# Optimization experiments

Hardware: AMD Instinct MI355X
Metric: run time of the kernel (lower is better)

## Reference

```python
import jax, jax.numpy as jnp
import numpy as np

N = 20000          # nodes
E = 320000         # edges (before self-loops)
H, C = 8, 32       # heads, hidden_size
ND, ED = 6, 11     # node_dim, edge_dim (hard-coded in module)
HC = H * C
DIFF_SCALE = 100.0
SLOPE = 0.2        # GATv2 leaky_relu negative_slope


def _glorot(k, shape):
    fan_in, fan_out = shape[0], shape[-1]
    lim = float(np.sqrt(6.0 / (fan_in + fan_out)))
    return jax.random.uniform(k, shape, jnp.float32, -lim, lim)


def setup_inputs() -> dict:
    key = jax.random.key(0)
    ks = jax.random.split(key, 16)
    d = {}
    d["x"] = jax.random.normal(ks[0], (N, ND), jnp.float32)
    d["edge_index"] = jax.random.randint(ks[1], (2, E), 0, N)
    d["edge_attr"] = jax.random.normal(ks[2], (E, ED), jnp.float32)
    # layer 0 (node_dim -> H*C, with edge features)
    d["Wl0"] = _glorot(ks[3], (ND, HC)); d["bl0"] = jnp.zeros((HC,), jnp.float32)
    d["Wr0"] = _glorot(ks[4], (ND, HC)); d["br0"] = jnp.zeros((HC,), jnp.float32)
    d["We0"] = _glorot(ks[5], (ED, HC))
    d["att0"] = _glorot(ks[6], (H, C))
    d["bias0"] = jnp.zeros((HC,), jnp.float32)
    # layer 1 (H*C -> H*C, no edge features)
    d["Wl1"] = _glorot(ks[7], (HC, HC)); d["bl1"] = jnp.zeros((HC,), jnp.float32)
    d["Wr1"] = _glorot(ks[8], (HC, HC)); d["br1"] = jnp.zeros((HC,), jnp.float32)
    d["att1"] = _glorot(ks[9], (H, C))
    d["bias1"] = jnp.zeros((HC,), jnp.float32)
    return d


def _gatv2(x, src, tgt, Wl, bl, Wr, br, att, bias, e=None, We=None):
    n = x.shape[0]
    xl = (x @ Wl + bl).reshape(n, H, C)   # source transform (messages)
    xr = (x @ Wr + br).reshape(n, H, C)   # target transform
    m = xl[src] + xr[tgt]                 # [E', H, C]
    if e is not None:
        m = m + (e @ We).reshape(-1, H, C)
    s = jax.nn.leaky_relu(m, SLOPE)
    logits = jnp.einsum('ehc,hc->eh', s, att)            # [E', H]
    # segment softmax over incoming edges of each target node
    mx = jax.ops.segment_max(logits, tgt, num_segments=n)
    ex = jnp.exp(logits - mx[tgt])
    den = jax.ops.segment_sum(ex, tgt, num_segments=n)
    alpha = ex / den[tgt]                                 # [E', H]
    out = jax.ops.segment_sum(alpha[:, :, None] * xl[src], tgt, num_segments=n)
    return out.reshape(n, HC) + bias


def reference(x, edge_index, edge_attr, Wl0, bl0, Wr0, br0, We0, att0, bias0,
              Wl1, bl1, Wr1, br1, att1, bias1):
    # preprocessing from GraphEmbedder.forward
    x = jnp.where((x[:, 2] == 1)[:, None] & (jnp.arange(ND) == 1)[None, :],
                  ((x[:, 1] - x[:, 0]) / DIFF_SCALE)[:, None], x)
    edge_attr = jnp.where((edge_attr[:, -2] == 1)[:, None] & (jnp.arange(ED) == 1)[None, :],
                          ((edge_attr[:, 1] - edge_attr[:, 0]) / DIFF_SCALE)[:, None], edge_attr)
    # add self-loops (PyG GATv2Conv default, fill_value='mean' for edge_attr)
    loop = jnp.arange(N)
    src = jnp.concatenate([edge_index[0], loop])
    tgt = jnp.concatenate([edge_index[1], loop])
    ea = jnp.concatenate([edge_attr, jnp.broadcast_to(edge_attr.mean(0), (N, ED))])
    h = _gatv2(x, src, tgt, Wl0, bl0, Wr0, br0, att0, bias0, e=ea, We=We0)
    h = jax.nn.elu(h)
    h = _gatv2(h, src, tgt, Wl1, bl1, Wr1, br1, att1, bias1)
    return h
```

## Files before the change

kernel.cpp:

```cpp
#include <hip/hip_runtime.h>
#include <cstddef>

#define N_H 8
#define N_C 32
#define N_HC 256
#define SLOPE 0.2f

__global__ __launch_bounds__(256) void ea_colsum_kernel(const float* __restrict__ ea,
                                                        float* __restrict__ sums, int E) {
    float loc[11];
#pragma unroll
    for (int j = 0; j < 11; ++j) loc[j] = 0.f;
    for (int i = blockIdx.x * blockDim.x + threadIdx.x; i < E; i += gridDim.x * blockDim.x) {
        float r[11];
#pragma unroll
        for (int j = 0; j < 11; ++j) r[j] = ea[i * 11 + j];
        if (r[9] == 1.0f) r[1] = (r[1] - r[0]) * 0.01f;
#pragma unroll
        for (int j = 0; j < 11; ++j) loc[j] += r[j];
    }
    __shared__ float sbuf[256];
#pragma unroll
    for (int j = 0; j < 11; ++j) {
        sbuf[threadIdx.x] = loc[j];
        __syncthreads();
        for (int s = 128; s > 0; s >>= 1) {
            if (threadIdx.x < s) sbuf[threadIdx.x] += sbuf[threadIdx.x + s];
            __syncthreads();
        }
        if (threadIdx.x == 0) atomicAdd(&sums[j], sbuf[0]);
        __syncthreads();
    }
}

__global__ void mean_div_kernel(const float* __restrict__ sums, float* __restrict__ mean, int E) {
    int t = threadIdx.x;
    if (t < 11) mean[t] = sums[t] / (float)E;
}

__global__ __launch_bounds__(256) void deg_hist_kernel(const int* __restrict__ ei,
                                                       int* __restrict__ deg, int E, int Etot) {
    int e = blockIdx.x * blockDim.x + threadIdx.x;
    if (e >= Etot) return;
    int t = (e < E) ? ei[E + e] : e - E;
    atomicAdd(&deg[t], 1);
}

__global__ __launch_bounds__(1024) void scan_kernel(const int* __restrict__ deg,
                                                    int* __restrict__ offs,
                                                    int* __restrict__ cursor, int Nn) {
    const int T = 1024;
    int tid = threadIdx.x;
    int chunk = (Nn + T - 1) / T;
    int b = tid * chunk;
    int s = 0;
    for (int k = 0; k < chunk; ++k) {
        int i = b + k;
        if (i < Nn) s += deg[i];
    }
    __shared__ int sm[T];
    sm[tid] = s;
    __syncthreads();
    for (int d = 1; d < T; d <<= 1) {
        int v = (tid >= d) ? sm[tid - d] : 0;
        __syncthreads();
        sm[tid] += v;
        __syncthreads();
    }
    int pref = (tid > 0) ? sm[tid - 1] : 0;
    for (int k = 0; k < chunk; ++k) {
        int i = b + k;
        if (i < Nn) {
            offs[i] = pref;
            cursor[i] = pref;
            pref += deg[i];
        }
    }
    if (tid == T - 1) offs[Nn] = sm[T - 1];
}

__global__ __launch_bounds__(256) void scatter_kernel(const int* __restrict__ ei,
                                                      const float* __restrict__ ea,
                                                      const float* __restrict__ mean_ea,
                                                      int* __restrict__ cursor,
                                                      int* __restrict__ esrc,
                                                      float* __restrict__ ea_csr, int E,
                                                      int Etot) {
    int e = blockIdx.x * blockDim.x + threadIdx.x;
    if (e >= Etot) return;
    int s, t;
    if (e < E) { s = ei[e]; t = ei[E + e]; }
    else       { s = t = e - E; }
    int pos = atomicAdd(&cursor[t], 1);
    esrc[pos] = s;
    float r[11];
    if (e < E) {
#pragma unroll
        for (int j = 0; j < 11; ++j) r[j] = ea[(size_t)e * 11 + j];
        if (r[9] == 1.0f) r[1] = (r[1] - r[0]) * 0.01f;
    } else {
#pragma unroll
        for (int j = 0; j < 11; ++j) r[j] = mean_ea[j];
    }
    float* dst = ea_csr + (size_t)pos * 12;
#pragma unroll
    for (int j = 0; j < 11; ++j) dst[j] = r[j];
}

template <int K, int R>
__global__ __launch_bounds__(256) void node_mm_kernel(const float* __restrict__ X,
                                                      const float* __restrict__ Wl,
                                                      const float* __restrict__ bl,
                                                      const float* __restrict__ Wr,
                                                      const float* __restrict__ br,
                                                      float* __restrict__ xl,
                                                      float* __restrict__ xr, int Nn) {
    __shared__ float xs[R][K];
    int row0 = blockIdx.x * R;
    int tid = threadIdx.x;
    for (int i = tid; i < R * K; i += blockDim.x) {
        int r = i / K, k = i - r * K;
        int gr = row0 + r;
        float v = 0.f;
        if (gr < Nn) {
            v = X[(size_t)gr * K + k];
            if (k == 1) {
                float x0 = X[(size_t)gr * K + 0];
                float x2 = X[(size_t)gr * K + 2];
                if (x2 == 1.0f) v = (v - x0) * 0.01f;
            }
        }
        xs[r][k] = v;
    }
    __syncthreads();
    int c = tid;
    float accl[R], accr[R];
#pragma unroll
    for (int r = 0; r < R; ++r) { accl[r] = bl[c]; accr[r] = br[c]; }
#pragma unroll
    for (int k = 0; k < K; ++k) {
        float wl = Wl[k * N_HC + c], wr = Wr[k * N_HC + c];
#pragma unroll
        for (int r = 0; r < R; ++r) {
            accl[r] = fmaf(xs[r][k], wl, accl[r]);
            accr[r] = fmaf(xs[r][k], wr, accr[r]);
        }
    }
#pragma unroll
    for (int r = 0; r < R; ++r) {
        int gr = row0 + r;
        if (gr < Nn) {
            xl[(size_t)gr * N_HC + c] = accl[r];
            xr[(size_t)gr * N_HC + c] = accr[r];
        }
    }
}

__global__ __launch_bounds__(256) void gemm256_kernel(const float* __restrict__ X,
                                                      const float* __restrict__ Wl,
                                                      const float* __restrict__ bl,
                                                      const float* __restrict__ Wr,
                                                      const float* __restrict__ br,
                                                      float* __restrict__ xl,
                                                      float* __restrict__ xr, int Nn) {
    __shared__ float As[32][128];
    __shared__ float Bs[32][128];

    const int by = blockIdx.y;
    const float* __restrict__ W = (by < 2) ? Wl : Wr;
    const float* __restrict__ bias = (by < 2) ? bl : br;
    float* __restrict__ dst = (by < 2) ? xl : xr;
    const int cb = (by & 1) * 128;
    const int row0 = blockIdx.x * 128;
    const int tid = threadIdx.x;
    const int tx = tid & 15, ty = tid >> 4;
    const int tx4 = tx * 4, ty4 = ty * 4;

    const int arow = tid & 127;
    const int akh = (tid >> 7) * 16;
    const int bk0 = tid >> 5;
    const int bc4 = (tid & 31) * 4;

    float acc[8][8];
#pragma unroll
    for (int i = 0; i < 8; ++i)
#pragma unroll
        for (int j = 0; j < 8; ++j) acc[i][j] = 0.f;

    const int garow = row0 + arow;
    const bool aval = garow < Nn;
    const float* __restrict__ asrc = X + (size_t)garow * 256 + akh;

    for (int s = 0; s < 256; s += 32) {
        float4 av[4];
#pragma unroll
        for (int q = 0; q < 4; ++q)
            av[q] = aval ? *(const float4*)(asrc + s + q * 4)
                         : float4{0.f, 0.f, 0.f, 0.f};
#pragma unroll
        for (int q = 0; q < 4; ++q) {
            As[akh + q * 4 + 0][arow] = av[q].x;
            As[akh + q * 4 + 1][arow] = av[q].y;
            As[akh + q * 4 + 2][arow] = av[q].z;
            As[akh + q * 4 + 3][arow] = av[q].w;
        }
#pragma unroll
        for (int q = 0; q < 4; ++q) {
            int kr = bk0 + q * 8;
            *(float4*)&Bs[kr][bc4] = *(const float4*)(W + (size_t)(s + kr) * 256 + cb + bc4);
        }
        __syncthreads();
#pragma unroll 8
        for (int k = 0; k < 32; ++k) {
            const float4 a0 = *(const float4*)&As[k][ty4];
            const float4 a1 = *(const float4*)&As[k][64 + ty4];
            const float4 b0 = *(const float4*)&Bs[k][tx4];
            const float4 b1 = *(const float4*)&Bs[k][64 + tx4];
            const float ar[8] = {a0.x, a0.y, a0.z, a0.w, a1.x, a1.y, a1.z, a1.w};
            const float brr[8] = {b0.x, b0.y, b0.z, b0.w, b1.x, b1.y, b1.z, b1.w};
#pragma unroll
            for (int i = 0; i < 8; ++i)
#pragma unroll
                for (int j = 0; j < 8; ++j) acc[i][j] = fmaf(ar[i], brr[j], acc[i][j]);
        }
        __syncthreads();
    }

    const float4 bv0 = *(const float4*)(bias + cb + tx4);
    const float4 bv1 = *(const float4*)(bias + cb + 64 + tx4);
#pragma unroll
    for (int i = 0; i < 8; ++i) {
        int r = row0 + ((i < 4) ? (ty4 + i) : (64 + ty4 + i - 4));
        if (r < Nn) {
            float4 v0 = {acc[i][0] + bv0.x, acc[i][1] + bv0.y, acc[i][2] + bv0.z,
                         acc[i][3] + bv0.w};
            float4 v1 = {acc[i][4] + bv1.x, acc[i][5] + bv1.y, acc[i][6] + bv1.z,
                         acc[i][7] + bv1.w};
            *(float4*)(dst + (size_t)r * N_HC + cb + tx4) = v0;
            *(float4*)(dst + (size_t)r * N_HC + cb + 64 + tx4) = v1;
        }
    }
}

__device__ __forceinline__ void online_update(float logit, const float4& xlv, float& m,
                                              float& den, float4& acc) {
    float mn = fmaxf(m, logit);
    float s = __expf(m - mn);
    float w = __expf(logit - mn);
    den = den * s + w;
    acc.x = fmaf(w, xlv.x, acc.x * s);
    acc.y = fmaf(w, xlv.y, acc.y * s);
    acc.z = fmaf(w, xlv.z, acc.z * s);
    acc.w = fmaf(w, xlv.w, acc.w * s);
    m = mn;
}

template <bool L0>
__device__ __forceinline__ float edge_logit(const float4& xlv, const float4& xrv,
                                            const float4* Wreg, const float* __restrict__ eap,
                                            const float4& av) {
    float m0 = xlv.x + xrv.x, m1 = xlv.y + xrv.y, m2 = xlv.z + xrv.z, m3 = xlv.w + xrv.w;
    if (L0) {
#pragma unroll
        for (int j = 0; j < 11; ++j) {
            float aj = eap[j];
            m0 = fmaf(aj, Wreg[j].x, m0);
            m1 = fmaf(aj, Wreg[j].y, m1);
            m2 = fmaf(aj, Wreg[j].z, m2);
            m3 = fmaf(aj, Wreg[j].w, m3);
        }
    }
    m0 = m0 > 0.f ? m0 : SLOPE * m0;
    m1 = m1 > 0.f ? m1 : SLOPE * m1;
    m2 = m2 > 0.f ? m2 : SLOPE * m2;
    m3 = m3 > 0.f ? m3 : SLOPE * m3;
    float p = m0 * av.x + m1 * av.y + m2 * av.z + m3 * av.w;
    p += __shfl_xor(p, 1);
    p += __shfl_xor(p, 2);
    p += __shfl_xor(p, 4);
    return p;
}

template <bool L0>
__global__ __launch_bounds__(256) void node_gather_kernel(
    const int* __restrict__ offs, const int* __restrict__ esrc,
    const float* __restrict__ ea_csr, const float* __restrict__ We,
    const float* __restrict__ att, const float* __restrict__ xl, const float* __restrict__ xr,
    const float* __restrict__ bias, float* __restrict__ out, int Nn) {
    int wid = threadIdx.x >> 6;
    int lane = threadIdx.x & 63;
    int node = blockIdx.x * 4 + wid;
    if (node >= Nn) return;
    int c4 = lane * 4;

    float4 Wreg[11];
    if (L0) {
#pragma unroll
        for (int j = 0; j < 11; ++j) Wreg[j] = *(const float4*)(We + j * N_HC + c4);
    }
    const float4 xrv = *(const float4*)(xr + (size_t)node * N_HC + c4);
    const float4 av = *(const float4*)(att + c4);

    int beg = offs[node], end = offs[node + 1];

    float mA = -INFINITY, dA = 0.f;
    float mB = -INFINITY, dB = 0.f;
    float mC = -INFINITY, dC = 0.f;
    float mD = -INFINITY, dD = 0.f;
    float4 aA = {0.f, 0.f, 0.f, 0.f}, aB = aA, aC = aA, aD = aA;

    int p = beg;
    for (; p + 3 < end; p += 4) {
        int pu = __builtin_amdgcn_readfirstlane(p);
        int s0 = esrc[pu + 0];
        int s1 = esrc[pu + 1];
        int s2 = esrc[pu + 2];
        int s3 = esrc[pu + 3];
        const float4 x0 = *(const float4*)(xl + (size_t)s0 * N_HC + c4);
        const float4 x1 = *(const float4*)(xl + (size_t)s1 * N_HC + c4);
        const float4 x2 = *(const float4*)(xl + (size_t)s2 * N_HC + c4);
        const float4 x3 = *(const float4*)(xl + (size_t)s3 * N_HC + c4);
        const float* e0 = L0 ? (ea_csr + (size_t)(pu + 0) * 12) : nullptr;
        const float* e1 = L0 ? (ea_csr + (size_t)(pu + 1) * 12) : nullptr;
        const float* e2 = L0 ? (ea_csr + (size_t)(pu + 2) * 12) : nullptr;
        const float* e3 = L0 ? (ea_csr + (size_t)(pu + 3) * 12) : nullptr;
        float lg0 = edge_logit<L0>(x0, xrv, Wreg, e0, av);
        float lg1 = edge_logit<L0>(x1, xrv, Wreg, e1, av);
        float lg2 = edge_logit<L0>(x2, xrv, Wreg, e2, av);
        float lg3 = edge_logit<L0>(x3, xrv, Wreg, e3, av);
        online_update(lg0, x0, mA, dA, aA);
        online_update(lg1, x1, mB, dB, aB);
        online_update(lg2, x2, mC, dC, aC);
        online_update(lg3, x3, mD, dD, aD);
    }
    for (; p < end; ++p) {
        int pu = __builtin_amdgcn_readfirstlane(p);
        int s0 = esrc[pu];
        const float4 x0 = *(const float4*)(xl + (size_t)s0 * N_HC + c4);
        const float* e0 = L0 ? (ea_csr + (size_t)pu * 12) : nullptr;
        float lg0 = edge_logit<L0>(x0, xrv, Wreg, e0, av);
        online_update(lg0, x0, mA, dA, aA);
    }

    float mm = fmaxf(fmaxf(mA, mB), fmaxf(mC, mD));
    float sA = __expf(mA - mm), sB = __expf(mB - mm);
    float sC = __expf(mC - mm), sD = __expf(mD - mm);
    float den = dA * sA + dB * sB + dC * sC + dD * sD;
    float4 acct;
    acct.x = aA.x * sA + aB.x * sB + aC.x * sC + aD.x * sD;
    acct.y = aA.y * sA + aB.y * sB + aC.y * sC + aD.y * sD;
    acct.z = aA.z * sA + aB.z * sB + aC.z * sC + aD.z * sD;
    acct.w = aA.w * sA + aB.w * sB + aC.w * sC + aD.w * sD;

    const float4 bv = *(const float4*)(bias + c4);
    float4 r;
    r.x = acct.x / den + bv.x;
    r.y = acct.y / den + bv.y;
    r.z = acct.z / den + bv.z;
    r.w = acct.w / den + bv.w;
    if (L0) {
        r.x = r.x > 0.f ? r.x : (__expf(r.x) - 1.f);
        r.y = r.y > 0.f ? r.y : (__expf(r.y) - 1.f);
        r.z = r.z > 0.f ? r.z : (__expf(r.z) - 1.f);
        r.w = r.w > 0.f ? r.w : (__expf(r.w) - 1.f);
    }
    *(float4*)(out + (size_t)node * N_HC + c4) = r;
}

extern "C" void kernel_launch(void* const* d_in, const int* in_sizes, int n_in, void* d_out,
                              int out_size, void* d_ws, size_t ws_size, hipStream_t stream) {
    const float* x = (const float*)d_in[0];
    const int* ei = (const int*)d_in[1];
    const float* ea = (const float*)d_in[2];
    const float* Wl0 = (const float*)d_in[3];
    const float* bl0 = (const float*)d_in[4];
    const float* Wr0 = (const float*)d_in[5];
    const float* br0 = (const float*)d_in[6];
    const float* We0 = (const float*)d_in[7];
    const float* att0 = (const float*)d_in[8];
    const float* bias0 = (const float*)d_in[9];
    const float* Wl1 = (const float*)d_in[10];
    const float* bl1 = (const float*)d_in[11];
    const float* Wr1 = (const float*)d_in[12];
    const float* br1 = (const float*)d_in[13];
    const float* att1 = (const float*)d_in[14];
    const float* bias1 = (const float*)d_in[15];
    float* out = (float*)d_out;

    const int Nn = in_sizes[0] / 6;
    const int E = in_sizes[1] / 2;
    const int Etot = E + Nn;

    auto align16 = [](size_t v) { return (v + 15) & ~(size_t)15; };
    float* ws = (float*)d_ws;
    size_t o = 0;
    float* xl = ws + o;     o = align16(o + (size_t)Nn * N_HC);
    float* xr = ws + o;     o = align16(o + (size_t)Nn * N_HC);
    float* h = ws + o;      o = align16(o + (size_t)Nn * N_HC);
    float* ea_csr = ws + o; o = align16(o + (size_t)Etot * 12);
    float* easum = ws + o;  o = align16(o + 16);
    float* mean = ws + o;   o = align16(o + 16);
    int* deg = (int*)(ws + o);    o = align16(o + (size_t)Nn);
    int* offs = (int*)(ws + o);   o = align16(o + (size_t)Nn + 1);
    int* cursor = (int*)(ws + o); o = align16(o + (size_t)Nn);
    int* esrc = (int*)(ws + o);   o = align16(o + (size_t)Etot);

    hipMemsetAsync(easum, 0, 16 * sizeof(float), stream);
    hipMemsetAsync(deg, 0, (size_t)Nn * sizeof(int), stream);

    ea_colsum_kernel<<<256, 256, 0, stream>>>(ea, easum, E);
    mean_div_kernel<<<1, 32, 0, stream>>>(easum, mean, E);

    deg_hist_kernel<<<(Etot + 255) / 256, 256, 0, stream>>>(ei, deg, E, Etot);
    scan_kernel<<<1, 1024, 0, stream>>>(deg, offs, cursor, Nn);
    scatter_kernel<<<(Etot + 255) / 256, 256, 0, stream>>>(ei, ea, mean, cursor, esrc, ea_csr, E,
                                                           Etot);

    const int gblocks = (Nn + 3) / 4;

    node_mm_kernel<6, 8><<<(Nn + 7) / 8, 256, 0, stream>>>(x, Wl0, bl0, Wr0, br0, xl, xr, Nn);
    node_gather_kernel<true><<<gblocks, 256, 0, stream>>>(offs, esrc, ea_csr, We0, att0, xl, xr,
                                                          bias0, h, Nn);

    dim3 ggrid((Nn + 127) / 128, 4);
    gemm256_kernel<<<ggrid, 256, 0, stream>>>(h, Wl1, bl1, Wr1, br1, xl, xr, Nn);
    node_gather_kernel<false><<<gblocks, 256, 0, stream>>>(offs, esrc, nullptr, nullptr, att1, xl,
                                                           xr, bias1, out, Nn);
}
```

Measured before the change: 322.8 us.

## Run layer-1 GEMM on bf16 MFMA with split hi/lo precision emulation

Replaces the FP32 SIMT GEMM for the 256x512 layer-1 projection with an MFMA bf16 kernel. Each operand is split into a bf16 high part and a residual low part, and three MFMA products are summed to approximate fp32 accuracy. This adds two conversion kernels and uses the output buffer as scratch for the converted activations. The MFMA kernel loads operands straight from global memory without LDS staging. Accuracy is somewhat below true fp32, and the extra conversion traffic could offset the gain from the faster matrix units.

Measured after the change: 347.4 us. 1.08x slower.

```diff
diff --git a/kernel.cpp b/kernel.cpp
--- a/kernel.cpp
+++ b/kernel.cpp
@@ -5,6 +5,18 @@
 #define N_C 32
 #define N_HC 256
 #define SLOPE 0.2f
+
+typedef __attribute__((ext_vector_type(8))) short short8v;
+typedef __attribute__((ext_vector_type(4))) float f32x4;
+
+__device__ __forceinline__ short f2bf(float f) {
+    unsigned u = __float_as_uint(f);
+    unsigned r = (u + 0x7FFFu + ((u >> 16) & 1u)) >> 16;
+    return (short)r;
+}
+__device__ __forceinline__ float bf2f(short s) {
+    return __uint_as_float(((unsigned)(unsigned short)s) << 16);
+}
 
 __global__ __launch_bounds__(256) void ea_colsum_kernel(const float* __restrict__ ea,
                                                         float* __restrict__ sums, int E) {
@@ -156,6 +168,98 @@
     }
 }
 
+__global__ __launch_bounds__(256) void convert_h_kernel(const float* __restrict__ h,
+                                                        short* __restrict__ Ahi,
+                                                        short* __restrict__ Alo, int n4) {
+    int i = blockIdx.x * blockDim.x + threadIdx.x;
+    if (i >= n4) return;
+    float4 v = ((const float4*)h)[i];
+    short h0 = f2bf(v.x), h1 = f2bf(v.y), h2 = f2bf(v.z), h3 = f2bf(v.w);
+    short4 hv = {h0, h1, h2, h3};
+    short4 lv = {f2bf(v.x - bf2f(h0)), f2bf(v.y - bf2f(h1)), f2bf(v.z - bf2f(h2)),
+                 f2bf(v.w - bf2f(h3))};
+    *(short4*)(Ahi + (size_t)i * 4) = hv;
+    *(short4*)(Alo + (size_t)i * 4) = lv;
+}
+
+__global__ __launch_bounds__(256) void convert_w_kernel(const float* __restrict__ Wl,
+                                                        const float* __restrict__ Wr,
+                                                        short* __restrict__ Bthi,
+                                                        short* __restrict__ Btlo) {
+    int n = blockIdx.x;
+    int k = threadIdx.x;
+    float v = (n < 256) ? Wl[(size_t)k * 256 + n] : Wr[(size_t)k * 256 + (n - 256)];
+    short hi = f2bf(v);
+    short lo = f2bf(v - bf2f(hi));
+    size_t idx = (size_t)n * 256 + k;
+    Bthi[idx] = hi;
+    Btlo[idx] = lo;
+}
+
+__global__ __launch_bounds__(256) void gemm_mfma_kernel(
+    const short* __restrict__ Ahi, const short* __restrict__ Alo,
+    const short* __restrict__ Bthi, const short* __restrict__ Btlo,
+    const float* __restrict__ bl, const float* __restrict__ br, float* __restrict__ xl,
+    float* __restrict__ xr, int Nn) {
+    const int wid = threadIdx.x >> 6, lane = threadIdx.x & 63;
+    const int lm = lane & 15, lg = lane >> 4;
+    const int r0 = blockIdx.x * 128 + wid * 32;
+    const int c0 = blockIdx.y * 64;
+    const int kg = lg * 8;
+
+    f32x4 acc[2][4];
+#pragma unroll
+    for (int i = 0; i < 2; ++i)
+#pragma unroll
+        for (int j = 0; j < 4; ++j) acc[i][j] = {0.f, 0.f, 0.f, 0.f};
+
+    const int rA0 = r0 + lm, rA1 = r0 + 16 + lm;
+    const bool v0 = rA0 < Nn, v1 = rA1 < Nn;
+    const short* pa0h = Ahi + (size_t)rA0 * 256 + kg;
+    const short* pa0l = Alo + (size_t)rA0 * 256 + kg;
+    const short* pa1h = Ahi + (size_t)rA1 * 256 + kg;
+    const short* pa1l = Alo + (size_t)rA1 * 256 + kg;
+    const size_t nb = (size_t)(c0 + lm) * 256 + kg;
+    const short8v zz = (short8v)0;
+
+    for (int k0 = 0; k0 < 256; k0 += 32) {
+        short8v a0h = v0 ? *(const short8v*)(pa0h + k0) : zz;
+        short8v a0l = v0 ? *(const short8v*)(pa0l + k0) : zz;
+        short8v a1h = v1 ? *(const short8v*)(pa1h + k0) : zz;
+        short8v a1l = v1 ? *(const short8v*)(pa1l + k0) : zz;
+#pragma unroll
+        for (int ni = 0; ni < 4; ++ni) {
+            const short8v bh = *(const short8v*)(Bthi + nb + (size_t)ni * 16 * 256 + k0);
+            const short8v blo = *(const short8v*)(Btlo + nb + (size_t)ni * 16 * 256 + k0);
+            acc[0][ni] = __builtin_amdgcn_mfma_f32_16x16x32_bf16(a0h, bh, acc[0][ni], 0, 0, 0);
+            acc[0][ni] = __builtin_amdgcn_mfma_f32_16x16x32_bf16(a0l, bh, acc[0][ni], 0, 0, 0);
+            acc[0][ni] = __builtin_amdgcn_mfma_f32_16x16x32_bf16(a0h, blo, acc[0][ni], 0, 0, 0);
+            acc[1][ni] = __builtin_amdgcn_mfma_f32_16x16x32_bf16(a1h, bh, acc[1][ni], 0, 0, 0);
+            acc[1][ni] = __builtin_amdgcn_mfma_f32_16x16x32_bf16(a1l, bh, acc[1][ni], 0, 0, 0);
+            acc[1][ni] = __builtin_amdgcn_mfma_f32_16x16x32_bf16(a1h, blo, acc[1][ni], 0, 0, 0);
+        }
+    }
+
+    const bool left = (c0 < 256);
+    const float* __restrict__ bias = left ? bl : br;
+    float* __restrict__ dst = left ? xl : xr;
+    const int cl = (c0 & 255) + lm;
+#pragma unroll
+    for (int ni = 0; ni < 4; ++ni) {
+        int col = cl + ni * 16;
+        float bv = bias[col];
+#pragma unroll
+        for (int mi = 0; mi < 2; ++mi) {
+            int rb = r0 + mi * 16 + lg * 4;
+#pragma unroll
+            for (int e = 0; e < 4; ++e) {
+                int row = rb + e;
+                if (row < Nn) dst[(size_t)row * N_HC + col] = acc[mi][ni][e] + bv;
+            }
+        }
+    }
+}
+
 __global__ __launch_bounds__(256) void gemm256_kernel(const float* __restrict__ X,
                                                       const float* __restrict__ Wl,
                                                       const float* __restrict__ bl,
@@ -195,8 +299,7 @@
         float4 av[4];
 #pragma unroll
         for (int q = 0; q < 4; ++q)
-            av[q] = aval ? *(const float4*)(asrc + s + q * 4)
-                         : float4{0.f, 0.f, 0.f, 0.f};
+            av[q] = aval ? *(const float4*)(asrc + s + q * 4) : float4{0.f, 0.f, 0.f, 0.f};
 #pragma unroll
         for (int q = 0; q < 4; ++q) {
             As[akh + q * 4 + 0][arow] = av[q].x;
@@ -232,12 +335,12 @@
     for (int i = 0; i < 8; ++i) {
         int r = row0 + ((i < 4) ? (ty4 + i) : (64 + ty4 + i - 4));
         if (r < Nn) {
-            float4 v0 = {acc[i][0] + bv0.x, acc[i][1] + bv0.y, acc[i][2] + bv0.z,
+            float4 u0 = {acc[i][0] + bv0.x, acc[i][1] + bv0.y, acc[i][2] + bv0.z,
                          acc[i][3] + bv0.w};
-            float4 v1 = {acc[i][4] + bv1.x, acc[i][5] + bv1.y, acc[i][6] + bv1.z,
+            float4 u1 = {acc[i][4] + bv1.x, acc[i][5] + bv1.y, acc[i][6] + bv1.z,
                          acc[i][7] + bv1.w};
-            *(float4*)(dst + (size_t)r * N_HC + cb + tx4) = v0;
-            *(float4*)(dst + (size_t)r * N_HC + cb + 64 + tx4) = v1;
+            *(float4*)(dst + (size_t)r * N_HC + cb + tx4) = u0;
+            *(float4*)(dst + (size_t)r * N_HC + cb + 64 + tx4) = u1;
         }
     }
 }
@@ -404,6 +507,9 @@
     int* offs = (int*)(ws + o);   o = align16(o + (size_t)Nn + 1);
     int* cursor = (int*)(ws + o); o = align16(o + (size_t)Nn);
     int* esrc = (int*)(ws + o);   o = align16(o + (size_t)Etot);
+    short* Bthi = (short*)(ws + o); o = align16(o + 512 * 256 / 2);
+    short* Btlo = (short*)(ws + o); o = align16(o + 512 * 256 / 2);
+    const bool use_mfma = (o * sizeof(float) <= ws_size);
 
     hipMemsetAsync(easum, 0, 16 * sizeof(float), stream);
     hipMemsetAsync(deg, 0, (size_t)Nn * sizeof(int), stream);
@@ -422,8 +528,18 @@
     node_gather_kernel<true><<<gblocks, 256, 0, stream>>>(offs, esrc, ea_csr, We0, att0, xl, xr,
                                                           bias0, h, Nn);
 
-    dim3 ggrid((Nn + 127) / 128, 4);
-    gemm256_kernel<<<ggrid, 256, 0, stream>>>(h, Wl1, bl1, Wr1, br1, xl, xr, Nn);
+    if (use_mfma) {
+        short* Ahi = (short*)d_out;
+        short* Alo = Ahi + (size_t)Nn * N_HC;
+        convert_h_kernel<<<(Nn * N_HC / 4 + 255) / 256, 256, 0, stream>>>(h, Ahi, Alo,
+                                                                          Nn * N_HC / 4);
+        convert_w_kernel<<<512, 256, 0, stream>>>(Wl1, Wr1, Bthi, Btlo);
+        dim3 mgrid((Nn + 127) / 128, 8);
+        gemm_mfma_kernel<<<mgrid, 256, 0, stream>>>(Ahi, Alo, Bthi, Btlo, bl1, br1, xl, xr, Nn);
+    } else {
+        dim3 ggrid((Nn + 127) / 128, 4);
+        gemm256_kernel<<<ggrid, 256, 0, stream>>>(h, Wl1, bl1, Wr1, br1, xl, xr, Nn);
+    }
     node_gather_kernel<false><<<gblocks, 256, 0, stream>>>(offs, esrc, nullptr, nullptr, att1, xl,
                                                            xr, bias1, out, Nn);
 }
```
